# Kernel tuning notes

Measured on AMD Instinct MI355X. Metric: run time of the kernel, lower is better.

The kernel has to match this reference:

```python
import jax, jax.numpy as jnp
import numpy as np


def _mlp(x, params):
    # params: list of (W, b); tanh on all layers except the last (linear head)
    h = x
    n = len(params)
    for i, (W, b) in enumerate(params):
        h = h @ W + b
        if i < n - 1:
            h = jnp.tanh(h)
    return h


def setup_inputs() -> dict:
    key = jax.random.key(0)
    D, H, B = 32, 256, 2048
    ks = jax.random.split(key, 13)

    def init_w(k, fan_in, fan_out):
        return jax.random.normal(k, (fan_in, fan_out), dtype=jnp.float32) / np.sqrt(fan_in)

    inp = {"x": jax.random.normal(ks[0], (B, D), dtype=jnp.float32)}
    # score net: D -> H -> H -> D
    inp["sW1"] = init_w(ks[1], D, H); inp["sb1"] = jnp.zeros((H,), jnp.float32)
    inp["sW2"] = init_w(ks[2], H, H); inp["sb2"] = jnp.zeros((H,), jnp.float32)
    inp["sW3"] = init_w(ks[3], H, D); inp["sb3"] = jnp.zeros((D,), jnp.float32)
    # covariance net: D -> H -> H -> D*D
    inp["cW1"] = init_w(ks[4], D, H); inp["cb1"] = jnp.zeros((H,), jnp.float32)
    inp["cW2"] = init_w(ks[5], H, H); inp["cb2"] = jnp.zeros((H,), jnp.float32)
    inp["cW3"] = init_w(ks[6], H, D * D); inp["cb3"] = jnp.zeros((D * D,), jnp.float32)
    return inp


def reference(x, sW1, sb1, sW2, sb2, sW3, sb3, cW1, cb1, cW2, cb2, cW3, cb3):
    B = x.shape[0]
    d = sW1.shape[0]
    sp = [(sW1, sb1), (sW2, sb2), (sW3, sb3)]
    cp = [(cW1, cb1), (cW2, cb2), (cW3, cb3)]

    # score and trace of its Jacobian (hutchinson_samples == 0 path)
    score = _mlp(x, sp)                                   # [B, d]
    score_fn = lambda xi: _mlp(xi, sp)
    Js = jax.vmap(jax.jacfwd(score_fn))(x)                # [B, d, d]
    jacobian_trace = jnp.trace(Js, axis1=1, axis2=2)      # [B]

    # covariance net and its divergence: cov_div[b, i] = sum_j d cov[b, i, j] / d x[b, j]
    cov = _mlp(x, cp).reshape(B, d, d)                    # [B, d, d]
    cov_fn = lambda xi: _mlp(xi, cp)
    Jc = jax.vmap(jax.jacfwd(cov_fn))(x).reshape(B, d, d, d)  # [B, i, j, j_in]
    cov_div = jnp.einsum('bijj->bi', Jc)                  # [B, d]

    return (score, jacobian_trace, cov, cov_div)
```

## Files before the change

kernel.cpp:

```cpp
#include <hip/hip_runtime.h>
#include <math.h>

#define Dd 32
#define Hh 256

using short8  = __attribute__((ext_vector_type(8))) short;
using floatx4 = __attribute__((ext_vector_type(4))) float;

__device__ inline unsigned short f2bf(float f) {
    union { float f; unsigned u; } v; v.f = f;
    unsigned r = (v.u + 0x7FFFu + ((v.u >> 16) & 1u)) >> 16;
    return (unsigned short)r;
}
__device__ inline float bf2f(unsigned short h) {
    union { unsigned u; float f; } v; v.u = ((unsigned)h) << 16;
    return v.f;
}

__global__ __launch_bounds__(256) void k1_prep(
    const float* __restrict__ sW1, const float* __restrict__ sW2, const float* __restrict__ sW3,
    const float* __restrict__ cW1, const float* __restrict__ cW2, const float* __restrict__ cW3,
    unsigned short* __restrict__ cW3t,
    unsigned short* __restrict__ sW2t, unsigned short* __restrict__ cW2t,
    unsigned short* __restrict__ sW3t,
    unsigned short* __restrict__ W1ts, unsigned short* __restrict__ W1tc)
{
    __shared__ float fl[64][33];
    const int tid = threadIdx.x;
    const int bid = blockIdx.x;

    if (bid < 49) {
        const float* src; unsigned short* dst; int stride, n0;
        if (bid < 32)      { src = cW3; dst = cW3t; stride = 1024; n0 = bid * 32; }
        else if (bid < 40) { src = sW2; dst = sW2t; stride = 256;  n0 = (bid - 32) * 32; }
        else if (bid < 48) { src = cW2; dst = cW2t; stride = 256;  n0 = (bid - 40) * 32; }
        else               { src = sW3; dst = sW3t; stride = 32;   n0 = 0; }

        const int nn  = tid & 31, kg = tid >> 5;
        const int nn2 = tid >> 3, ks = (tid & 7) * 8;

        for (int p = 0; p < 4; ++p) {
            if (p) __syncthreads();
            #pragma unroll
            for (int j = 0; j < 8; ++j) {
                int kk = kg * 8 + j;
                fl[kk][nn] = src[(size_t)(p * 64 + kk) * stride + n0 + nn];
            }
            __syncthreads();
            short8 v;
            #pragma unroll
            for (int j = 0; j < 8; ++j) v[j] = (short)f2bf(fl[ks + j][nn2]);
            *(short8*)(dst + (size_t)(n0 + nn2) * 256 + p * 64 + ks) = v;
        }
        return;
    }
    {
        const float* W1 = (bid == 49) ? sW1 : cW1;
        unsigned short* dst = (bid == 49) ? W1ts : W1tc;
        const int n = tid;
        #pragma unroll
        for (int c = 0; c < 4; ++c) {
            short8 v;
            #pragma unroll
            for (int j = 0; j < 8; ++j)
                v[j] = (short)f2bf(W1[(size_t)(c * 8 + j) * 256 + n]);
            *(short8*)(dst + (size_t)n * 32 + c * 8) = v;
        }
    }
}

__global__ __launch_bounds__(256) void ka_mfma(
    const float* __restrict__ x,
    const float* __restrict__ sW1, const float* __restrict__ sW2, const float* __restrict__ sW3,
    const float* __restrict__ cW1, const float* __restrict__ cW2, const float* __restrict__ cW3,
    const unsigned short* __restrict__ W1ts, const unsigned short* __restrict__ W1tc,
    const unsigned short* __restrict__ sW2t, const unsigned short* __restrict__ cW2t,
    const unsigned short* __restrict__ sW3t,
    const float* __restrict__ sb1, const float* __restrict__ sb2, const float* __restrict__ sb3,
    const float* __restrict__ cb1, const float* __restrict__ cb2,
    float* __restrict__ out_score,
    unsigned short* __restrict__ T1s, unsigned short* __restrict__ T2s,
    unsigned short* __restrict__ T1c, unsigned short* __restrict__ T2c,
    unsigned short* __restrict__ H2c, unsigned short* __restrict__ Mt)
{
    __shared__ char smem[9216];
    const int tid = threadIdx.x;
    const int bid = blockIdx.x;

    if (bid >= 256) {
        const int pb = bid - 256;
        const int kq = pb & 3;
        const int i  = pb >> 2;
        float (*W1t)[36] = (float(*)[36])smem;

        const float *W1, *W2, *C3;
        int cstride, coff;
        if (i == 0) { W1 = sW1; W2 = sW2; C3 = sW3; cstride = 32;   coff = 0; }
        else        { W1 = cW1; W2 = cW2; C3 = cW3; cstride = 1024; coff = (i - 1) * 32; }

        {
            int kl = tid & 63, jg = tid >> 6;
            #pragma unroll
            for (int jj = 0; jj < 8; ++jj) {
                int j = jg * 8 + jj;
                W1t[kl][j] = W1[j * 256 + kq * 64 + kl];
            }
        }
        float ct[32];
        {
            const float* src = C3 + (size_t)tid * cstride + coff;
            #pragma unroll
            for (int j4 = 0; j4 < 8; ++j4) {
                float4 v = *(const float4*)(src + j4 * 4);
                ct[j4 * 4 + 0] = v.x; ct[j4 * 4 + 1] = v.y;
                ct[j4 * 4 + 2] = v.z; ct[j4 * 4 + 3] = v.w;
            }
        }
        __syncthreads();

        for (int kg = 0; kg < 8; ++kg) {
            const int kbase = kq * 64 + kg * 8;
            short8 pk;
            #pragma unroll
            for (int q = 0; q < 8; ++q) {
                float a = 0.f;
                #pragma unroll
                for (int j4 = 0; j4 < 8; ++j4) {
                    float4 w = *(const float4*)&W1t[kg * 8 + q][j4 * 4];
                    a += w.x * ct[j4 * 4 + 0] + w.y * ct[j4 * 4 + 1]
                       + w.z * ct[j4 * 4 + 2] + w.w * ct[j4 * 4 + 3];
                }
                float m = a * W2[(size_t)(kbase + q) * 256 + tid];
                pk[q] = (short)f2bf(m);
            }
            *(short8*)(Mt + (size_t)i * 65536 + (size_t)tid * 256 + kbase) = pk;
        }
        return;
    }

    const int net = bid & 1;
    const int sb  = (bid >> 1) * 16;

    const unsigned short* W1t = net ? W1tc : W1ts;
    const unsigned short* W2t = net ? cW2t : sW2t;
    const float* b1 = net ? cb1 : sb1;
    const float* b2 = net ? cb2 : sb2;
    unsigned short* T1 = net ? T1c : T1s;
    unsigned short* T2 = net ? T2c : T2s;

    unsigned short (*hB)[264] = (unsigned short(*)[264])smem;

    const int w    = tid >> 6;
    const int lane = tid & 63;
    const int g    = lane >> 4;
    const int r16  = lane & 15;

    short8 ax;
    {
        const float* xs = x + (size_t)(sb + r16) * 32 + g * 8;
        float4 a = *(const float4*)xs;
        float4 b = *(const float4*)(xs + 4);
        ax[0] = (short)f2bf(a.x); ax[1] = (short)f2bf(a.y);
        ax[2] = (short)f2bf(a.z); ax[3] = (short)f2bf(a.w);
        ax[4] = (short)f2bf(b.x); ax[5] = (short)f2bf(b.y);
        ax[6] = (short)f2bf(b.z); ax[7] = (short)f2bf(b.w);
    }

    #pragma unroll
    for (int nt = 0; nt < 4; ++nt) {
        const int nb = w * 64 + nt * 16;
        short8 bf = *(const short8*)(W1t + (size_t)(nb + r16) * 32 + g * 8);
        floatx4 acc = (floatx4){0.f, 0.f, 0.f, 0.f};
        acc = __builtin_amdgcn_mfma_f32_16x16x32_bf16(ax, bf, acc, 0, 0, 0);
        const float bias = b1[nb + r16];
        #pragma unroll
        for (int reg = 0; reg < 4; ++reg) {
            float h = tanhf(acc[reg] + bias);
            int m = g * 4 + reg;
            hB[m][nb + r16] = f2bf(h);
            T1[(size_t)(sb + m) * 256 + nb + r16] = f2bf(1.0f - h * h);
        }
    }
    __syncthreads();

    short8 bfr[8];
    #pragma unroll
    for (int ks = 0; ks < 8; ++ks)
        bfr[ks] = *(const short8*)&hB[r16][ks * 32 + g * 8];

    unsigned short h2st[4][4];
    #pragma unroll
    for (int mt = 0; mt < 4; ++mt) {
        const int cb = w * 64 + mt * 16;
        floatx4 acc = (floatx4){0.f, 0.f, 0.f, 0.f};
        #pragma unroll
        for (int ks = 0; ks < 8; ++ks) {
            short8 af = *(const short8*)(W2t + (size_t)(cb + r16) * 256 + ks * 32 + g * 8);
            acc = __builtin_amdgcn_mfma_f32_16x16x32_bf16(af, bfr[ks], acc, 0, 0, 0);
        }
        #pragma unroll
        for (int reg = 0; reg < 4; ++reg) {
            const int c2 = cb + g * 4 + reg;
            float h = tanhf(acc[reg] + b2[c2]);
            unsigned short hb = f2bf(h);
            T2[(size_t)(sb + r16) * 256 + c2] = f2bf(1.0f - h * h);
            if (net) H2c[(size_t)(sb + r16) * 256 + c2] = hb;
            h2st[mt][reg] = hb;
        }
    }

    if (!net) {
        __syncthreads();
        #pragma unroll
        for (int mt = 0; mt < 4; ++mt)
            #pragma unroll
            for (int reg = 0; reg < 4; ++reg)
                hB[r16][w * 64 + mt * 16 + g * 4 + reg] = h2st[mt][reg];
        __syncthreads();

        if (w < 2) {
            floatx4 acc = (floatx4){0.f, 0.f, 0.f, 0.f};
            #pragma unroll
            for (int ks = 0; ks < 8; ++ks) {
                short8 af = *(const short8*)(sW3t + (size_t)(w * 16 + r16) * 256 + ks * 32 + g * 8);
                short8 bf = *(const short8*)&hB[r16][ks * 32 + g * 8];
                acc = __builtin_amdgcn_mfma_f32_16x16x32_bf16(af, bf, acc, 0, 0, 0);
            }
            #pragma unroll
            for (int reg = 0; reg < 4; ++reg) {
                const int m = w * 16 + g * 4 + reg;
                out_score[(size_t)(sb + r16) * 32 + m] = acc[reg] + sb3[m];
            }
        }
    }
}

__global__ __launch_bounds__(256, 2) void kb_mfma(
    const unsigned short* __restrict__ T1s, const unsigned short* __restrict__ T2s,
    const unsigned short* __restrict__ T1c, const unsigned short* __restrict__ T2c,
    const unsigned short* __restrict__ H2c,
    const unsigned short* __restrict__ Mt,  const unsigned short* __restrict__ cW3t,
    const float* __restrict__ cb3,
    float* __restrict__ out_trace, float* __restrict__ out_cdiv,
    float* __restrict__ out_cov)
{
    const int stile = blockIdx.x;
    const int job   = blockIdx.y;
    const int sbase = stile * 64;
    const bool contr = (job < 33);

    const unsigned short* A  = contr ? (job == 0 ? T1s : T1c) : H2c;
    const unsigned short* Bm = contr ? (Mt + (size_t)job * 65536)
                                     : (cW3t + (size_t)(job - 33) * 65536);
    const unsigned short* T2 = (job == 0) ? T2s : T2c;

    __shared__ unsigned short Bs[2][128 * 64];
    __shared__ float red[4][64];

    const int tid  = threadIdx.x;
    const int w    = tid >> 6;
    const int lane = tid & 63;
    const int g    = lane >> 4;
    const int r16  = lane & 15;

    short8 af[4][8];
    #pragma unroll
    for (int mt = 0; mt < 4; ++mt)
        #pragma unroll
        for (int c = 0; c < 8; ++c)
            af[mt][c] = *(const short8*)(A + (size_t)(sbase + mt * 16 + r16) * 256
                                           + c * 32 + g * 8);

    const int tl   = tid >> 1;
    const int kseg = tid & 1;

    short8 st[4];
    {
        const unsigned short* src = Bm + (size_t)tl * 256 + kseg * 32;
        #pragma unroll
        for (int j = 0; j < 4; ++j) st[j] = *(const short8*)(src + j * 8);
    }

    float pp[4][4];
    #pragma unroll
    for (int mt = 0; mt < 4; ++mt)
        #pragma unroll
        for (int reg = 0; reg < 4; ++reg) pp[mt][reg] = 0.f;

    floatx4 acc[4][2];

    for (int idx = 0; idx < 8; ++idx) {
        const int buf = idx & 1;
        const int c4  = idx & 3;
        const int sec = idx >> 2;

        #pragma unroll
        for (int j = 0; j < 4; ++j)
            *(short8*)&Bs[buf][tl * 64 + ((kseg * 4 + j + tl) & 7) * 8] = st[j];

        if (idx < 7) {
            const int ni = idx + 1;
            const unsigned short* src = Bm + (size_t)((ni >> 2) * 128 + tl) * 256
                                           + (ni & 3) * 64 + kseg * 32;
            #pragma unroll
            for (int j = 0; j < 4; ++j) st[j] = *(const short8*)(src + j * 8);
        }

        if (c4 == 0) {
            #pragma unroll
            for (int mt = 0; mt < 4; ++mt)
                #pragma unroll
                for (int nt = 0; nt < 2; ++nt)
                    acc[mt][nt] = (floatx4){0.f, 0.f, 0.f, 0.f};
        }

        #pragma unroll
        for (int kk = 0; kk < 2; ++kk) {
            #pragma unroll
            for (int nt = 0; nt < 2; ++nt) {
                const int row = w * 32 + nt * 16 + r16;
                short8 bfr = *(const short8*)&Bs[buf][row * 64 + ((kk * 4 + g + row) & 7) * 8];
                #pragma unroll
                for (int mt = 0; mt < 4; ++mt)
                    acc[mt][nt] = __builtin_amdgcn_mfma_f32_16x16x32_bf16(
                        af[mt][c4 * 2 + kk], bfr, acc[mt][nt], 0, 0, 0);
            }
        }

        if (c4 == 3) {
            if (contr) {
                #pragma unroll
                for (int mt = 0; mt < 4; ++mt)
                    #pragma unroll
                    for (int nt = 0; nt < 2; ++nt)
                        #pragma unroll
                        for (int reg = 0; reg < 4; ++reg) {
                            int r = mt * 16 + g * 4 + reg;
                            int t = sec * 128 + w * 32 + nt * 16 + r16;
                            pp[mt][reg] += acc[mt][nt][reg]
                                         * bf2f(T2[(size_t)(sbase + r) * 256 + t]);
                        }
            } else {
                const int n0 = (job - 33) * 256;
                #pragma unroll
                for (int mt = 0; mt < 4; ++mt)
                    #pragma unroll
                    for (int nt = 0; nt < 2; ++nt) {
                        int n = sec * 128 + w * 32 + nt * 16 + r16;
                        float bias = cb3[n0 + n];
                        #pragma unroll
                        for (int reg = 0; reg < 4; ++reg) {
                            int r = mt * 16 + g * 4 + reg;
                            out_cov[(size_t)(sbase + r) * 1024 + n0 + n] = acc[mt][nt][reg] + bias;
                        }
                    }
            }
        }
    }

    if (contr) {
        #pragma unroll
        for (int mt = 0; mt < 4; ++mt)
            #pragma unroll
            for (int reg = 0; reg < 4; ++reg) {
                float v = pp[mt][reg];
                v += __shfl_xor(v, 1, 64);
                v += __shfl_xor(v, 2, 64);
                v += __shfl_xor(v, 4, 64);
                v += __shfl_xor(v, 8, 64);
                pp[mt][reg] = v;
            }
        if (r16 == 0) {
            #pragma unroll
            for (int mt = 0; mt < 4; ++mt)
                #pragma unroll
                for (int reg = 0; reg < 4; ++reg)
                    red[w][mt * 16 + g * 4 + reg] = pp[mt][reg];
        }
        __syncthreads();
        if (tid < 64) {
            float v = red[0][tid] + red[1][tid] + red[2][tid] + red[3][tid];
            int sg = sbase + tid;
            if (job == 0) out_trace[sg] = v;
            else          out_cdiv[(size_t)sg * Dd + (job - 1)] = v;
        }
    }
}

extern "C" void kernel_launch(void* const* d_in, const int* in_sizes, int n_in,
                              void* d_out, int out_size, void* d_ws, size_t ws_size,
                              hipStream_t stream) {
    const float* x   = (const float*)d_in[0];
    const float* sW1 = (const float*)d_in[1];
    const float* sb1 = (const float*)d_in[2];
    const float* sW2 = (const float*)d_in[3];
    const float* sb2 = (const float*)d_in[4];
    const float* sW3 = (const float*)d_in[5];
    const float* sb3 = (const float*)d_in[6];
    const float* cW1 = (const float*)d_in[7];
    const float* cb1 = (const float*)d_in[8];
    const float* cW2 = (const float*)d_in[9];
    const float* cb2 = (const float*)d_in[10];
    const float* cW3 = (const float*)d_in[11];
    const float* cb3 = (const float*)d_in[12];

    const int B = in_sizes[0] / Dd;

    float* out       = (float*)d_out;
    float* out_score = out;
    float* out_trace = out + (size_t)B * Dd;
    float* out_cov   = out_trace + B;
    float* out_cdiv  = out_cov + (size_t)B * Dd * Dd;

    unsigned short* ws16 = (unsigned short*)d_ws;
    const size_t SZ = (size_t)B * 256;
    unsigned short* T1s  = ws16;
    unsigned short* T2s  = ws16 + SZ;
    unsigned short* T1c  = ws16 + 2 * SZ;
    unsigned short* T2c  = ws16 + 3 * SZ;
    unsigned short* H2c  = ws16 + 4 * SZ;
    unsigned short* Mt   = ws16 + 5 * SZ;
    unsigned short* cW3t = Mt + (size_t)33 * 65536;
    unsigned short* sW2t = cW3t + (size_t)1024 * 256;
    unsigned short* cW2t = sW2t + (size_t)256 * 256;
    unsigned short* sW3t = cW2t + (size_t)256 * 256;
    unsigned short* W1ts = sW3t + (size_t)32 * 256;
    unsigned short* W1tc = W1ts + (size_t)256 * 32;

    k1_prep<<<dim3(51), dim3(256), 0, stream>>>(
        sW1, sW2, sW3, cW1, cW2, cW3,
        cW3t, sW2t, cW2t, sW3t, W1ts, W1tc);

    ka_mfma<<<dim3(256 + 132), dim3(256), 0, stream>>>(
        x, sW1, sW2, sW3, cW1, cW2, cW3,
        W1ts, W1tc, sW2t, cW2t, sW3t,
        sb1, sb2, sb3, cb1, cb2,
        out_score, T1s, T2s, T1c, T2c, H2c, Mt);

    kb_mfma<<<dim3(B / 64, 37), dim3(256), 0, stream>>>(
        T1s, T2s, T1c, T2c, H2c, Mt, cW3t, cb3,
        out_trace, out_cdiv, out_cov);
}
```

Baseline: 142.4 us.

## Pre-swizzle operands into MFMA fragment layout and drop LDS staging in kb

Weights, T1/T2/H2c intermediates and the M tensors are now written in a fragment-tiled layout, so each lane can load its MFMA operand as one contiguous short8 straight from global memory. The B-matrix double buffer in shared memory and the register prefetch loop in kb_mfma are removed. Each wave now computes a 64x64 accumulator tile directly from global/L2 loads, and T2 is read in 4-wide vectors that match the accumulator layout. Launch bounds are raised to 3 blocks per CU. The aim is to cut LDS traffic, barriers and uncoalesced loads, at the cost of more accumulator registers and more reliance on cache hits for the B operand.

```diff
diff --git a/kernel.cpp b/kernel.cpp
--- a/kernel.cpp
+++ b/kernel.cpp
@@ -4,8 +4,9 @@
 #define Dd 32
 #define Hh 256
 
-using short8  = __attribute__((ext_vector_type(8))) short;
-using floatx4 = __attribute__((ext_vector_type(4))) float;
+using short8   = __attribute__((ext_vector_type(8))) short;
+using floatx4  = __attribute__((ext_vector_type(4))) float;
+typedef unsigned short ushort4v __attribute__((ext_vector_type(4)));
 
 __device__ inline unsigned short f2bf(float f) {
     union { float f; unsigned u; } v; v.f = f;
@@ -15,6 +16,11 @@
 __device__ inline float bf2f(unsigned short h) {
     union { unsigned u; float f; } v; v.u = ((unsigned)h) << 16;
     return v.f;
+}
+
+__device__ inline size_t offFrag256(int row, int k) {
+    return ((size_t)((row >> 4) * 8 + (k >> 5))) * 512
+         + (((k & 31) >> 3) * 16 + (row & 15)) * 8 + (k & 7);
 }
 
 __global__ __launch_bounds__(256) void k1_prep(
@@ -50,7 +56,8 @@
             short8 v;
             #pragma unroll
             for (int j = 0; j < 8; ++j) v[j] = (short)f2bf(fl[ks + j][nn2]);
-            *(short8*)(dst + (size_t)(n0 + nn2) * 256 + p * 64 + ks) = v;
+            const int k0 = p * 64 + ks;
+            *(short8*)(dst + offFrag256(n0 + nn2, k0)) = v;
         }
         return;
     }
@@ -59,12 +66,12 @@
         unsigned short* dst = (bid == 49) ? W1ts : W1tc;
         const int n = tid;
         #pragma unroll
-        for (int c = 0; c < 4; ++c) {
+        for (int c8 = 0; c8 < 4; ++c8) {
             short8 v;
             #pragma unroll
             for (int j = 0; j < 8; ++j)
-                v[j] = (short)f2bf(W1[(size_t)(c * 8 + j) * 256 + n]);
-            *(short8*)(dst + (size_t)n * 32 + c * 8) = v;
+                v[j] = (short)f2bf(W1[(size_t)(c8 * 8 + j) * 256 + n]);
+            *(short8*)(dst + (size_t)(n >> 4) * 512 + (c8 * 16 + (n & 15)) * 8) = v;
         }
     }
 }
@@ -133,7 +140,7 @@
                 float m = a * W2[(size_t)(kbase + q) * 256 + tid];
                 pk[q] = (short)f2bf(m);
             }
-            *(short8*)(Mt + (size_t)i * 65536 + (size_t)tid * 256 + kbase) = pk;
+            *(short8*)(Mt + (size_t)i * 65536 + offFrag256(tid, kbase)) = pk;
         }
         return;
     }
@@ -169,7 +176,7 @@
     #pragma unroll
     for (int nt = 0; nt < 4; ++nt) {
         const int nb = w * 64 + nt * 16;
-        short8 bf = *(const short8*)(W1t + (size_t)(nb + r16) * 32 + g * 8);
+        short8 bf = *(const short8*)(W1t + (size_t)(w * 4 + nt) * 512 + lane * 8);
         floatx4 acc = (floatx4){0.f, 0.f, 0.f, 0.f};
         acc = __builtin_amdgcn_mfma_f32_16x16x32_bf16(ax, bf, acc, 0, 0, 0);
         const float bias = b1[nb + r16];
@@ -177,8 +184,9 @@
         for (int reg = 0; reg < 4; ++reg) {
             float h = tanhf(acc[reg] + bias);
             int m = g * 4 + reg;
-            hB[m][nb + r16] = f2bf(h);
-            T1[(size_t)(sb + m) * 256 + nb + r16] = f2bf(1.0f - h * h);
+            int k = nb + r16;
+            hB[m][k] = f2bf(h);
+            T1[(size_t)(sb >> 4) * 4096 + offFrag256(m, k)] = f2bf(1.0f - h * h);
         }
     }
     __syncthreads();
@@ -187,6 +195,9 @@
     #pragma unroll
     for (int ks = 0; ks < 8; ++ks)
         bfr[ks] = *(const short8*)&hB[r16][ks * 32 + g * 8];
+
+    const int stile64 = sb >> 6;
+    const int mt64    = (sb >> 4) & 3;
 
     unsigned short h2st[4][4];
     #pragma unroll
@@ -195,7 +206,7 @@
         floatx4 acc = (floatx4){0.f, 0.f, 0.f, 0.f};
         #pragma unroll
         for (int ks = 0; ks < 8; ++ks) {
-            short8 af = *(const short8*)(W2t + (size_t)(cb + r16) * 256 + ks * 32 + g * 8);
+            short8 af = *(const short8*)(W2t + (size_t)((w * 4 + mt) * 8 + ks) * 512 + lane * 8);
             acc = __builtin_amdgcn_mfma_f32_16x16x32_bf16(af, bfr[ks], acc, 0, 0, 0);
         }
         #pragma unroll
@@ -203,8 +214,11 @@
             const int c2 = cb + g * 4 + reg;
             float h = tanhf(acc[reg] + b2[c2]);
             unsigned short hb = f2bf(h);
-            T2[(size_t)(sb + r16) * 256 + c2] = f2bf(1.0f - h * h);
-            if (net) H2c[(size_t)(sb + r16) * 256 + c2] = hb;
+            T2[(size_t)stile64 * 16384
+               + (size_t)(mt64 * 16 + (c2 >> 4)) * 256
+               + ((c2 & 15) + (r16 >> 2) * 16) * 4 + (r16 & 3)] = f2bf(1.0f - h * h);
+            if (net)
+                H2c[(size_t)(sb >> 4) * 4096 + offFrag256(r16, c2)] = hb;
             h2st[mt][reg] = hb;
         }
     }
@@ -222,7 +236,7 @@
             floatx4 acc = (floatx4){0.f, 0.f, 0.f, 0.f};
             #pragma unroll
             for (int ks = 0; ks < 8; ++ks) {
-                short8 af = *(const short8*)(sW3t + (size_t)(w * 16 + r16) * 256 + ks * 32 + g * 8);
+                short8 af = *(const short8*)(sW3t + (size_t)(w * 8 + ks) * 512 + lane * 8);
                 short8 bf = *(const short8*)&hB[r16][ks * 32 + g * 8];
                 acc = __builtin_amdgcn_mfma_f32_16x16x32_bf16(af, bf, acc, 0, 0, 0);
             }
@@ -235,7 +249,7 @@
     }
 }
 
-__global__ __launch_bounds__(256, 2) void kb_mfma(
+__global__ __launch_bounds__(256, 3) void kb_mfma(
     const unsigned short* __restrict__ T1s, const unsigned short* __restrict__ T2s,
     const unsigned short* __restrict__ T1c, const unsigned short* __restrict__ T2c,
     const unsigned short* __restrict__ H2c,
@@ -249,12 +263,11 @@
     const int sbase = stile * 64;
     const bool contr = (job < 33);
 
-    const unsigned short* A  = contr ? (job == 0 ? T1s : T1c) : H2c;
-    const unsigned short* Bm = contr ? (Mt + (size_t)job * 65536)
-                                     : (cW3t + (size_t)(job - 33) * 65536);
-    const unsigned short* T2 = (job == 0) ? T2s : T2c;
-
-    __shared__ unsigned short Bs[2][128 * 64];
+    const unsigned short* A   = contr ? (job == 0 ? T1s : T1c) : H2c;
+    const unsigned short* Bm  = contr ? (Mt + (size_t)job * 65536)
+                                      : (cW3t + (size_t)(job - 33) * 65536);
+    const unsigned short* T2f = (job == 0) ? T2s : T2c;
+
     __shared__ float red[4][64];
 
     const int tid  = threadIdx.x;
@@ -262,103 +275,49 @@
     const int lane = tid & 63;
     const int g    = lane >> 4;
     const int r16  = lane & 15;
-
-    short8 af[4][8];
+    const int st4  = stile * 4;
+
+    floatx4 acc[4][4];
     #pragma unroll
     for (int mt = 0; mt < 4; ++mt)
         #pragma unroll
-        for (int c = 0; c < 8; ++c)
-            af[mt][c] = *(const short8*)(A + (size_t)(sbase + mt * 16 + r16) * 256
-                                           + c * 32 + g * 8);
-
-    const int tl   = tid >> 1;
-    const int kseg = tid & 1;
-
-    short8 st[4];
-    {
-        const unsigned short* src = Bm + (size_t)tl * 256 + kseg * 32;
-        #pragma unroll
-        for (int j = 0; j < 4; ++j) st[j] = *(const short8*)(src + j * 8);
-    }
-
-    float pp[4][4];
+        for (int nt = 0; nt < 4; ++nt)
+            acc[mt][nt] = (floatx4){0.f, 0.f, 0.f, 0.f};
+
     #pragma unroll
-    for (int mt = 0; mt < 4; ++mt)
-        #pragma unroll
-        for (int reg = 0; reg < 4; ++reg) pp[mt][reg] = 0.f;
-
-    floatx4 acc[4][2];
-
-    for (int idx = 0; idx < 8; ++idx) {
-        const int buf = idx & 1;
-        const int c4  = idx & 3;
-        const int sec = idx >> 2;
-
-        #pragma unroll
-        for (int j = 0; j < 4; ++j)
-            *(short8*)&Bs[buf][tl * 64 + ((kseg * 4 + j + tl) & 7) * 8] = st[j];
-
-        if (idx < 7) {
-            const int ni = idx + 1;
-            const unsigned short* src = Bm + (size_t)((ni >> 2) * 128 + tl) * 256
-                                           + (ni & 3) * 64 + kseg * 32;
-            #pragma unroll
-            for (int j = 0; j < 4; ++j) st[j] = *(const short8*)(src + j * 8);
-        }
-
-        if (c4 == 0) {
-            #pragma unroll
-            for (int mt = 0; mt < 4; ++mt)
+    for (int c = 0; c < 8; ++c) {
+        short8 af[4], bf[4];
+        #pragma unroll
+        for (int mt = 0; mt < 4; ++mt)
+            af[mt] = *(const short8*)(A + (size_t)((st4 + mt) * 8 + c) * 512 + lane * 8);
+        #pragma unroll
+        for (int nt = 0; nt < 4; ++nt)
+            bf[nt] = *(const short8*)(Bm + (size_t)((w * 4 + nt) * 8 + c) * 512 + lane * 8);
+        #pragma unroll
+        for (int mt = 0; mt < 4; ++mt)
+            #pragma unroll
+            for (int nt = 0; nt < 4; ++nt)
+                acc[mt][nt] = __builtin_amdgcn_mfma_f32_16x16x32_bf16(af[mt], bf[nt], acc[mt][nt], 0, 0, 0);
+    }
+
+    if (contr) {
+        float pp[4][4];
+        #pragma unroll
+        for (int mt = 0; mt < 4; ++mt)
+            #pragma unroll
+            for (int reg = 0; reg < 4; ++reg) pp[mt][reg] = 0.f;
+
+        #pragma unroll
+        for (int mt = 0; mt < 4; ++mt)
+            #pragma unroll
+            for (int nt = 0; nt < 4; ++nt) {
+                ushort4v t2q = *(const ushort4v*)(T2f + (size_t)stile * 16384
+                                 + (size_t)((mt * 16 + (w * 4 + nt)) * 64 + lane) * 4);
                 #pragma unroll
-                for (int nt = 0; nt < 2; ++nt)
-                    acc[mt][nt] = (floatx4){0.f, 0.f, 0.f, 0.f};
-        }
-
-        #pragma unroll
-        for (int kk = 0; kk < 2; ++kk) {
-            #pragma unroll
-            for (int nt = 0; nt < 2; ++nt) {
-                const int row = w * 32 + nt * 16 + r16;
-                short8 bfr = *(const short8*)&Bs[buf][row * 64 + ((kk * 4 + g + row) & 7) * 8];
-                #pragma unroll
-                for (int mt = 0; mt < 4; ++mt)
-                    acc[mt][nt] = __builtin_amdgcn_mfma_f32_16x16x32_bf16(
-                        af[mt][c4 * 2 + kk], bfr, acc[mt][nt], 0, 0, 0);
-            }
-        }
-
-        if (c4 == 3) {
-            if (contr) {
-                #pragma unroll
-                for (int mt = 0; mt < 4; ++mt)
-                    #pragma unroll
-                    for (int nt = 0; nt < 2; ++nt)
-                        #pragma unroll
-                        for (int reg = 0; reg < 4; ++reg) {
-                            int r = mt * 16 + g * 4 + reg;
-                            int t = sec * 128 + w * 32 + nt * 16 + r16;
-                            pp[mt][reg] += acc[mt][nt][reg]
-                                         * bf2f(T2[(size_t)(sbase + r) * 256 + t]);
-                        }
-            } else {
-                const int n0 = (job - 33) * 256;
-                #pragma unroll
-                for (int mt = 0; mt < 4; ++mt)
-                    #pragma unroll
-                    for (int nt = 0; nt < 2; ++nt) {
-                        int n = sec * 128 + w * 32 + nt * 16 + r16;
-                        float bias = cb3[n0 + n];
-                        #pragma unroll
-                        for (int reg = 0; reg < 4; ++reg) {
-                            int r = mt * 16 + g * 4 + reg;
-                            out_cov[(size_t)(sbase + r) * 1024 + n0 + n] = acc[mt][nt][reg] + bias;
-                        }
-                    }
-            }
-        }
-    }
-
-    if (contr) {
+                for (int reg = 0; reg < 4; ++reg)
+                    pp[mt][reg] += acc[mt][nt][reg] * bf2f(t2q[reg]);
+            }
+
         #pragma unroll
         for (int mt = 0; mt < 4; ++mt)
             #pragma unroll
@@ -384,6 +343,20 @@
             if (job == 0) out_trace[sg] = v;
             else          out_cdiv[(size_t)sg * Dd + (job - 1)] = v;
         }
+    } else {
+        const int n0 = (job - 33) * 256;
+        #pragma unroll
+        for (int mt = 0; mt < 4; ++mt)
+            #pragma unroll
+            for (int nt = 0; nt < 4; ++nt) {
+                const int n = (w * 4 + nt) * 16 + r16;
+                const float bias = cb3[n0 + n];
+                #pragma unroll
+                for (int reg = 0; reg < 4; ++reg) {
+                    const int r = mt * 16 + g * 4 + reg;
+                    out_cov[(size_t)(sbase + r) * 1024 + n0 + n] = acc[mt][nt][reg] + bias;
+                }
+            }
     }
 }
 
```

Measured after the change: 121.7 us. 14.5% less time.
